# Performance work log

Hardware: AMD Instinct MI355X
Metric: run time of the kernel (lower is better)

The kernel has to match this reference:

```python
import jax, jax.numpy as jnp
import numpy as np

T, B, A, OBS = 128, 16, 32, 256
K, NACT, HID = 3, 9, 32


def setup_inputs() -> dict:
    key = jax.random.key(0)
    ks = jax.random.split(key, 12)
    sc = 0.1  # small init scale for stability
    d = {}
    d["x"] = jax.random.normal(ks[0], (T, B, A, OBS), jnp.float32)
    d["done"] = jax.random.randint(ks[1], (T, B), 0, 2, jnp.int32)
    d["actions"] = jax.random.randint(ks[2], (T, B, A, K), 0, NACT, jnp.int32)
    d["W1"] = sc * jax.random.normal(ks[3], (128, OBS), jnp.float32)
    d["b1"] = jnp.zeros((128,), jnp.float32)
    d["W2"] = sc * jax.random.normal(ks[4], (128, 128), jnp.float32)
    d["b2"] = jnp.zeros((128,), jnp.float32)
    d["W3"] = sc * jax.random.normal(ks[5], (64, 128), jnp.float32)
    d["b3"] = jnp.zeros((64,), jnp.float32)
    d["Wih"] = sc * jax.random.normal(ks[6], (4 * HID, 64), jnp.float32)
    d["Whh"] = sc * jax.random.normal(ks[7], (4 * HID, HID), jnp.float32)
    d["bih"] = jnp.zeros((4 * HID,), jnp.float32)
    d["bhh"] = jnp.zeros((4 * HID,), jnp.float32)
    d["Wh"] = sc * jax.random.normal(ks[8], (K, NACT, HID), jnp.float32)
    d["bh"] = jnp.zeros((K, NACT), jnp.float32)
    d["h0"] = jnp.zeros((B * A, HID), jnp.float32)
    d["c0"] = jnp.zeros((B * A, HID), jnp.float32)
    return d


def _forward(x, done, actions, W1, b1, W2, b2, W3, b3,
             Wih, Whh, bih, bhh, Wh, bh, h0, c0):
    # MLP trunk: n_obs -> 128 -> 128 -> 64 (tanh, tanh, linear)
    z = jnp.tanh(x @ W1.T + b1)
    z = jnp.tanh(z @ W2.T + b2)
    z = z @ W3.T + b3                       # [T, B, A, 64]
    zf = z.reshape(T, B * A, 64)
    # done[t] repeated per agent (repeat_interleave along batch*agent axis)
    done_f = jnp.repeat(done.astype(x.dtype), A, axis=1)  # [T, B*A]

    def step(carry, inp):
        h, c = carry
        zt, dt = inp                        # [B*A,64], [B*A]
        mask = (1.0 - dt)[:, None]
        h = h * mask
        c = c * mask
        gates = zt @ Wih.T + bih + h @ Whh.T + bhh  # [B*A, 4H]
        i, f, g, o = jnp.split(gates, 4, axis=-1)   # PyTorch gate order i,f,g,o
        i, f, o = jax.nn.sigmoid(i), jax.nn.sigmoid(f), jax.nn.sigmoid(o)
        g = jnp.tanh(g)
        c = f * c + i * g
        h = o * jnp.tanh(c)
        return (h, c), h

    (_, _), ys = jax.lax.scan(step, (h0, c0), (zf, done_f))
    y = ys.reshape(T, B, A, HID)
    # multi-head categorical logits: stacked heads [K, NACT, HID]
    logits = jnp.einsum('tbah,knh->tbakn', y, Wh) + bh  # [T,B,A,K,NACT]
    lp = jax.nn.log_softmax(logits, axis=-1)
    entropies = -jnp.sum(jnp.exp(lp) * lp, axis=-1)     # [T,B,A,K]
    alp = jnp.take_along_axis(lp, actions[..., None], axis=-1)[..., 0]  # [T,B,A,K]
    logprobs = jnp.prod(alp, axis=-1)  # faithful: product of per-head log-probs
    return logprobs, entropies


def reference(x, done, actions, W1, b1, W2, b2, W3, b3,
              Wih, Whh, bih, bhh, Wh, bh, h0, c0):
    logprobs, entropies = _forward(x, done, actions, W1, b1, W2, b2, W3, b3,
                                   Wih, Whh, bih, bhh, Wh, bh, h0, c0)
    return actions, logprobs, entropies
```

## Files before the change

### kernel.cpp

```cpp
#include <hip/hip_runtime.h>
#include <math.h>

namespace {
constexpr int Tn = 128, Bn = 16, An = 32, OBS = 256, Kh = 3, NACT = 9, HID = 32;
constexpr int TBA = Tn * Bn * An;
constexpr int BA  = Bn * An;
constexpr int OUT_LP  = TBA * Kh;
constexpr int OUT_ENT = TBA * Kh + TBA;
constexpr int NCHUNK = 32;
constexpr int CHUNKW = Tn / NCHUNK;

typedef __fp16   pk16x2 __attribute__((ext_vector_type(2)));
typedef _Float16 half8v __attribute__((ext_vector_type(8)));
typedef float    f32x4  __attribute__((ext_vector_type(4)));
}

__device__ __forceinline__ float fast_sig(float x) {
  return __builtin_amdgcn_rcpf(1.f + __expf(-x));
}
__device__ __forceinline__ float fast_tanh(float x) {
  return fmaf(2.f, fast_sig(2.f * x), -1.f);
}
__device__ __forceinline__ unsigned h2bits(pk16x2 h) {
  return __builtin_bit_cast(unsigned, h);
}
__device__ __forceinline__ pk16x2 bits2h(unsigned u) {
  return __builtin_bit_cast(pk16x2, u);
}
__device__ __forceinline__ int first_done_ge(unsigned long long dm0,
                                             unsigned long long dm1, int n) {
  unsigned long long m0 = (n < 64) ? (dm0 & (~0ull << n)) : 0ull;
  unsigned long long m1 = (n < 64) ? dm1 : (dm1 & (~0ull << (n - 64)));
  if (m0) return __builtin_ctzll(m0);
  if (m1) return 64 + __builtin_ctzll(m1);
  return 128;
}
__device__ __forceinline__ void bmax3(float& m0, float& m1, float& m2,
                                      int km, float v) {
  m0 = (km == 0) ? fmaxf(m0, v) : m0;
  m1 = (km == 1) ? fmaxf(m1, v) : m1;
  m2 = (km == 2) ? fmaxf(m2, v) : m2;
}
__device__ __forceinline__ void badd3(float& s0, float& s1, float& s2,
                                      int km, float v) {
  s0 += (km == 0) ? v : 0.f;
  s1 += (km == 1) ? v : 0.f;
  s2 += (km == 2) ? v : 0.f;
}
__device__ __forceinline__ float bsel3(float x0, float x1, float x2, int km) {
  return (km == 0) ? x0 : ((km == 1) ? x1 : x2);
}
__device__ __forceinline__ int bseli3(int x0, int x1, int x2, int km) {
  return (km == 0) ? x0 : ((km == 1) ? x1 : x2);
}

template<int ROWS, int WSTR>
__device__ __forceinline__ void stage_whf(const float* __restrict__ Wg, int kofs,
                                          _Float16* __restrict__ wt, int tid)
{
#pragma unroll
  for (int it = 0; it < ROWS/64; ++it) {
    int idx = tid + it*512;
    int o = idx >> 3, g8 = idx & 7;
    const float* p = &Wg[(size_t)o*WSTR + kofs + g8*8];
    float4 c0 = *(const float4*)p;
    float4 c1 = *(const float4*)(p + 4);
    half8v hv = { (_Float16)c0.x, (_Float16)c0.y, (_Float16)c0.z, (_Float16)c0.w,
                  (_Float16)c1.x, (_Float16)c1.y, (_Float16)c1.z, (_Float16)c1.w };
    *(half8v*)&wt[o*72 + g8*8] = hv;
  }
}

template<int NOC, int XSTR>
__device__ __forceinline__ void mfma_slab(const _Float16* __restrict__ xsrc,
                                          const _Float16* __restrict__ wt,
                                          int rA, int ln, int quad, f32x4 acc[8])
{
#pragma unroll
  for (int kc = 0; kc < 2; ++kc) {
    half8v a = *(const half8v*)&xsrc[rA*XSTR + kc*32 + quad*8];
#pragma unroll
    for (int oc = 0; oc < NOC; ++oc) {
      half8v b = *(const half8v*)&wt[(oc*16 + ln)*72 + kc*32 + quad*8];
      acc[oc] = __builtin_amdgcn_mfma_f32_16x16x32_f16(a, b, acc[oc], 0, 0, 0);
    }
  }
}

template<int NOC>
__device__ __forceinline__ void mfma_regA(half8v a0, half8v a1,
                                          const _Float16* __restrict__ wt,
                                          int ln, int quad, f32x4 acc[8])
{
#pragma unroll
  for (int oc = 0; oc < NOC; ++oc) {
    half8v b = *(const half8v*)&wt[(oc*16 + ln)*72 + quad*8];
    acc[oc] = __builtin_amdgcn_mfma_f32_16x16x32_f16(a0, b, acc[oc], 0, 0, 0);
  }
#pragma unroll
  for (int oc = 0; oc < NOC; ++oc) {
    half8v b = *(const half8v*)&wt[(oc*16 + ln)*72 + 32 + quad*8];
    acc[oc] = __builtin_amdgcn_mfma_f32_16x16x32_f16(a1, b, acc[oc], 0, 0, 0);
  }
}

__global__ __launch_bounds__(512, 4) void mlp_kernel(
    const float* __restrict__ x,
    const float* __restrict__ W1, const float* __restrict__ W2,
    const float* __restrict__ W3, const float* __restrict__ Wih,
    const float* __restrict__ b1, const float* __restrict__ b2,
    const float* __restrict__ b3, const float* __restrict__ bih,
    const float* __restrict__ bhh, uint2* __restrict__ G1q)
{
  __shared__ __align__(16) _Float16 wt0[128*72];
  __shared__ __align__(16) _Float16 wt1[128*72];
  __shared__ __align__(16) _Float16 act[128*136];
  const int tid  = threadIdx.x;
  const int w    = tid >> 6;
  const int lane = tid & 63;
  const int ln   = lane & 15;
  const int quad = lane >> 4;
  const int rA   = 16*w + ln;
  const int r0   = 16*w + quad*4;
  const int R0   = blockIdx.x * 128;
  f32x4 acc[8];
  const float* xrow = &x[(size_t)(R0 + rA)*OBS + quad*8];

#define XLOAD(KT, U0, U1, U2, U3) {                                   \
    const float* xp_ = xrow + (KT)*64;                                \
    U0 = *(const float4*)(xp_);      U1 = *(const float4*)(xp_ + 4);  \
    U2 = *(const float4*)(xp_ + 32); U3 = *(const float4*)(xp_ + 36); }
#define XCVT(U0, U1, U2, U3, A0, A1) {                                         \
    A0 = (half8v){(_Float16)U0.x,(_Float16)U0.y,(_Float16)U0.z,(_Float16)U0.w, \
                  (_Float16)U1.x,(_Float16)U1.y,(_Float16)U1.z,(_Float16)U1.w};\
    A1 = (half8v){(_Float16)U2.x,(_Float16)U2.y,(_Float16)U2.z,(_Float16)U2.w, \
                  (_Float16)U3.x,(_Float16)U3.y,(_Float16)U3.z,(_Float16)U3.w}; }

  float4 u0, u1, u2, u3, v0, v1, v2, v3;
  half8v a0, a1;

  XLOAD(0, u0, u1, u2, u3);
  stage_whf<128, 256>(W1, 0, wt0, tid);
#pragma unroll
  for (int oc = 0; oc < 8; ++oc) acc[oc] = (f32x4)0.f;
  __syncthreads();

  stage_whf<128, 256>(W1, 64, wt1, tid);
  XLOAD(1, v0, v1, v2, v3);
  XCVT(u0, u1, u2, u3, a0, a1);
  mfma_regA<8>(a0, a1, wt0, ln, quad, acc);
  __syncthreads();

  stage_whf<128, 256>(W1, 128, wt0, tid);
  XLOAD(2, u0, u1, u2, u3);
  XCVT(v0, v1, v2, v3, a0, a1);
  mfma_regA<8>(a0, a1, wt1, ln, quad, acc);
  __syncthreads();

  stage_whf<128, 256>(W1, 192, wt1, tid);
  XLOAD(3, v0, v1, v2, v3);
  XCVT(u0, u1, u2, u3, a0, a1);
  mfma_regA<8>(a0, a1, wt0, ln, quad, acc);
  __syncthreads();

  stage_whf<128, 128>(W2, 0, wt0, tid);
  XCVT(v0, v1, v2, v3, a0, a1);
  mfma_regA<8>(a0, a1, wt1, ln, quad, acc);
  __syncthreads();

#pragma unroll
  for (int oc = 0; oc < 8; ++oc) {
    int o = oc*16 + ln;
    float bv = b1[o];
#pragma unroll
    for (int r = 0; r < 4; ++r)
      act[(r0 + r)*136 + o] = (_Float16)fast_tanh(acc[oc][r] + bv);
  }

#pragma unroll
  for (int oc = 0; oc < 8; ++oc) acc[oc] = (f32x4)0.f;
  stage_whf<128, 128>(W2, 64, wt1, tid);
  mfma_slab<8, 136>(act, wt0, rA, ln, quad, acc);
  __syncthreads();

  stage_whf<64, 128>(W3, 0, wt0, tid);
  mfma_slab<8, 136>(act + 64, wt1, rA, ln, quad, acc);
  __syncthreads();

#pragma unroll
  for (int oc = 0; oc < 8; ++oc) {
    int o = oc*16 + ln;
    float bv = b2[o];
#pragma unroll
    for (int r = 0; r < 4; ++r)
      act[(r0 + r)*136 + o] = (_Float16)fast_tanh(acc[oc][r] + bv);
  }

#pragma unroll
  for (int oc = 0; oc < 4; ++oc) acc[oc] = (f32x4)0.f;
  stage_whf<64, 128>(W3, 64, wt1, tid);
  mfma_slab<4, 136>(act, wt0, rA, ln, quad, acc);
  __syncthreads();

  stage_whf<128, 64>(Wih, 0, wt0, tid);
  mfma_slab<4, 136>(act + 64, wt1, rA, ln, quad, acc);
  __syncthreads();

#pragma unroll
  for (int oc = 0; oc < 4; ++oc) {
    int o = oc*16 + ln;
    float bv = b3[o];
#pragma unroll
    for (int r = 0; r < 4; ++r)
      act[(r0 + r)*136 + o] = (_Float16)(acc[oc][r] + bv);
  }

#pragma unroll
  for (int oc = 0; oc < 8; ++oc) acc[oc] = (f32x4)0.f;
  mfma_slab<8, 136>(act, wt0, rA, ln, quad, acc);
#pragma unroll
  for (int p = 0; p < 2; ++p) {
    int ui = p*16 + ln;
    float bi = bih[ui]      + bhh[ui];
    float bf = bih[ui + 32] + bhh[ui + 32];
    float bg = bih[ui + 64] + bhh[ui + 64];
    float bo = bih[ui + 96] + bhh[ui + 96];
#pragma unroll
    for (int r = 0; r < 4; ++r) {
      int n = R0 + r0 + r;
      uint2 q;
      q.x = h2bits(__builtin_amdgcn_cvt_pkrtz(acc[p  ][r] + bi, acc[p+4][r] + bg));
      q.y = h2bits(__builtin_amdgcn_cvt_pkrtz(acc[p+2][r] + bf, acc[p+6][r] + bo));
      G1q[(size_t)n*32 + ui] = q;
    }
  }
#undef XLOAD
#undef XCVT
}

__global__ __launch_bounds__(64) void lstm_kernel(
    const uint2* __restrict__ G1q, const float* __restrict__ Whh,
    const float* __restrict__ Wh, const float* __restrict__ bh,
    const int* __restrict__ done, const int* __restrict__ actions,
    const float* __restrict__ h0, const float* __restrict__ c0,
    float* __restrict__ out)
{
  static_assert(BA == 512 && NCHUNK == 32, "index math below assumes 512x32");
  const int lane = threadIdx.x;
  const int ln   = lane & 15;
  const int q    = lane >> 4;
  const int rg   = blockIdx.x & 31;
  const int ck   = blockIdx.x >> 5;
  const int R0   = rg * 16;
  const int b    = R0 >> 5;

  const unsigned long long dm0 = __ballot(done[lane*Bn + b] != 0);
  const unsigned long long dm1 = __ballot(done[(lane + 64)*Bn + b] != 0);

  const int s = (ck == 0) ? 0 : first_done_ge(dm0, dm1, ck * CHUNKW);
  const int e = (ck == NCHUNK - 1) ? Tn
                                   : first_done_ge(dm0, dm1, (ck + 1) * CHUNKW);
  if (s >= e) return;

#define WFRAG(DST, ROWBASE, SRC, STRIDE, SCALE) {                              \
    const float* p_ = &(SRC)[(size_t)((ROWBASE) + ln)*(STRIDE) + q*8];         \
    float4 c0_ = *(const float4*)p_;                                           \
    float4 c1_ = *(const float4*)(p_ + 4);                                     \
    DST = (half8v){                                                            \
      (_Float16)(c0_.x*(SCALE)), (_Float16)(c0_.y*(SCALE)),                    \
      (_Float16)(c0_.z*(SCALE)), (_Float16)(c0_.w*(SCALE)),                    \
      (_Float16)(c1_.x*(SCALE)), (_Float16)(c1_.y*(SCALE)),                    \
      (_Float16)(c1_.z*(SCALE)), (_Float16)(c1_.w*(SCALE))}; }

  half8v wA0, wA1, wA2, wA3, wA4, wA5, wA6, wA7;
  WFRAG(wA0,   0, Whh, HID, 1.f)  WFRAG(wA1,  16, Whh, HID, 1.f)
  WFRAG(wA2,  32, Whh, HID, 1.f)  WFRAG(wA3,  48, Whh, HID, 1.f)
  WFRAG(wA4,  64, Whh, HID, 1.f)  WFRAG(wA5,  80, Whh, HID, 1.f)
  WFRAG(wA6,  96, Whh, HID, 1.f)  WFRAG(wA7, 112, Whh, HID, 1.f)

  half8v whA0, whA1;
  WFRAG(whA0, 0, Wh, HID, 1.f)
  {
    int row = 16 + ln;
    int rc  = (row < 27) ? row : 0;
    float zf = (row < 27) ? 1.f : 0.f;
    const float* p_ = &Wh[(size_t)rc*HID + q*8];
    float4 c0_ = *(const float4*)p_;
    float4 c1_ = *(const float4*)(p_ + 4);
    whA1 = (half8v){
      (_Float16)(c0_.x*zf), (_Float16)(c0_.y*zf),
      (_Float16)(c0_.z*zf), (_Float16)(c0_.w*zf),
      (_Float16)(c1_.x*zf), (_Float16)(c1_.y*zf),
      (_Float16)(c1_.z*zf), (_Float16)(c1_.w*zf)};
  }

  f32x4 bc0, bc1;
#pragma unroll
  for (int r = 0; r < 4; ++r) {
    int m0 = 4*q + r;
    int m1 = 16 + 4*q + r;
    bc0[r] = bh[m0];
    bc1[r] = (m1 < 27) ? bh[m1] : -1e30f;
  }

#define KOF(M, K, O) int K = (M)/9; K = (K > 2) ? 2 : K; const int O = (M) - 9*K;
  const int mA = 4*q, mB = 16 + 4*q;
  KOF(mA+0, kA0, oA0) KOF(mA+1, kA1, oA1) KOF(mA+2, kA2, oA2) KOF(mA+3, kA3, oA3)
  KOF(mB+0, kB0, oB0) KOF(mB+1, kB1, oB1) KOF(mB+2, kB2, oB2) KOF(mB+3, kB3, oB3)
#undef KOF

  const float4 z4 = {0.f, 0.f, 0.f, 0.f};
  float4 cs0, cs1;
  unsigned w0, w1, w2, w3;
  if (ck == 0) {
    const float* hp = &h0[(size_t)(R0 + ln)*HID + 4*q];
    const float* cp = &c0[(size_t)(R0 + ln)*HID + 4*q];
    float4 ha = *(const float4*)hp;
    float4 hb = *(const float4*)(hp + 16);
    cs0 = *(const float4*)cp;
    cs1 = *(const float4*)(cp + 16);
    w0 = h2bits(__builtin_amdgcn_cvt_pkrtz(ha.x, ha.y));
    w1 = h2bits(__builtin_amdgcn_cvt_pkrtz(ha.z, ha.w));
    w2 = h2bits(__builtin_amdgcn_cvt_pkrtz(hb.x, hb.y));
    w3 = h2bits(__builtin_amdgcn_cvt_pkrtz(hb.z, hb.w));
  } else {
    cs0 = z4; cs1 = z4;
    w0 = w1 = w2 = w3 = 0u;
  }

  const int aA = (ln + ((q & 1) << 5)) << 2;
  const int aB = aA + (16 << 2);
  const bool loq = (q < 2);

#define BBUILD(DST) {                                                      \
    unsigned e0_ = (unsigned)__builtin_amdgcn_ds_bpermute(aA, (int)w0);    \
    unsigned e1_ = (unsigned)__builtin_amdgcn_ds_bpermute(aA, (int)w1);    \
    unsigned e2_ = (unsigned)__builtin_amdgcn_ds_bpermute(aA, (int)w2);    \
    unsigned e3_ = (unsigned)__builtin_amdgcn_ds_bpermute(aA, (int)w3);    \
    unsigned o0_ = (unsigned)__builtin_amdgcn_ds_bpermute(aB, (int)w0);    \
    unsigned o1_ = (unsigned)__builtin_amdgcn_ds_bpermute(aB, (int)w1);    \
    unsigned o2_ = (unsigned)__builtin_amdgcn_ds_bpermute(aB, (int)w2);    \
    unsigned o3_ = (unsigned)__builtin_amdgcn_ds_bpermute(aB, (int)w3);    \
    uint4 bu_;                                                             \
    bu_.x = loq ? e0_ : e2_;  bu_.y = loq ? e1_ : e3_;                     \
    bu_.z = loq ? o0_ : o2_;  bu_.w = loq ? o1_ : o3_;                     \
    DST = __builtin_bit_cast(half8v, bu_); }

  half8v Bprev;
  if (ck == 0) { BBUILD(Bprev) }
  else {
    uint4 zz; zz.x = zz.y = zz.z = zz.w = 0u;
    Bprev = __builtin_bit_cast(half8v, zz);
  }

  const uint2* gb = G1q + ((size_t)(R0 + ln) * 32 + 4*q);
  const size_t gstep = (size_t)BA * 32;

#define LOADG(T, A0, A1, A2, A3)                                  \
  { const uint2* p_ = gb + (size_t)(T) * gstep;                   \
    A0 = *(const uint4*)(p_);      A1 = *(const uint4*)(p_ + 2);  \
    A2 = *(const uint4*)(p_ + 16); A3 = *(const uint4*)(p_ + 18); }

  uint4 rc0, rc1, rc2, rc3;
  LOADG(s, rc0, rc1, rc2, rc3);

  for (int t = s; t < e; ++t) {
    int tn = (t + 1 < e) ? t + 1 : e - 1;
    uint4 rn0, rn1, rn2, rn3;
    LOADG(tn, rn0, rn1, rn2, rn3);

    const int rowG = t*BA + R0 + ln;
    const int* ap = actions + (size_t)rowG*3;
    int a0 = ap[0], a1 = ap[1], a2 = ap[2];

    unsigned long long dbit = (t < 64) ? (dm0 >> t) : (dm1 >> (t - 64));
    half8v Buse = Bprev;
    if (dbit & 1ull) {
      uint4 zz; zz.x = zz.y = zz.z = zz.w = 0u;
      Buse = __builtin_bit_cast(half8v, zz);
      cs0 = z4; cs1 = z4;
    }

    f32x4 ci0, cf0, cg0, co0, ci1, cf1, cg1, co1;
    {
      pk16x2 ig, fo;
      ig = bits2h(rc0.x); fo = bits2h(rc0.y);
      ci0[0] = ig.x; cg0[0] = ig.y; cf0[0] = fo.x; co0[0] = fo.y;
      ig = bits2h(rc0.z); fo = bits2h(rc0.w);
      ci0[1] = ig.x; cg0[1] = ig.y; cf0[1] = fo.x; co0[1] = fo.y;
      ig = bits2h(rc1.x); fo = bits2h(rc1.y);
      ci0[2] = ig.x; cg0[2] = ig.y; cf0[2] = fo.x; co0[2] = fo.y;
      ig = bits2h(rc1.z); fo = bits2h(rc1.w);
      ci0[3] = ig.x; cg0[3] = ig.y; cf0[3] = fo.x; co0[3] = fo.y;
      ig = bits2h(rc2.x); fo = bits2h(rc2.y);
      ci1[0] = ig.x; cg1[0] = ig.y; cf1[0] = fo.x; co1[0] = fo.y;
      ig = bits2h(rc2.z); fo = bits2h(rc2.w);
      ci1[1] = ig.x; cg1[1] = ig.y; cf1[1] = fo.x; co1[1] = fo.y;
      ig = bits2h(rc3.x); fo = bits2h(rc3.y);
      ci1[2] = ig.x; cg1[2] = ig.y; cf1[2] = fo.x; co1[2] = fo.y;
      ig = bits2h(rc3.z); fo = bits2h(rc3.w);
      ci1[3] = ig.x; cg1[3] = ig.y; cf1[3] = fo.x; co1[3] = fo.y;
    }

    f32x4 ai0 = __builtin_amdgcn_mfma_f32_16x16x32_f16(wA0, Buse, ci0, 0, 0, 0);
    f32x4 ai1 = __builtin_amdgcn_mfma_f32_16x16x32_f16(wA1, Buse, ci1, 0, 0, 0);
    f32x4 af0 = __builtin_amdgcn_mfma_f32_16x16x32_f16(wA2, Buse, cf0, 0, 0, 0);
    f32x4 af1 = __builtin_amdgcn_mfma_f32_16x16x32_f16(wA3, Buse, cf1, 0, 0, 0);
    f32x4 ag0 = __builtin_amdgcn_mfma_f32_16x16x32_f16(wA4, Buse, cg0, 0, 0, 0);
    f32x4 ag1 = __builtin_amdgcn_mfma_f32_16x16x32_f16(wA5, Buse, cg1, 0, 0, 0);
    f32x4 ao0 = __builtin_amdgcn_mfma_f32_16x16x32_f16(wA6, Buse, co0, 0, 0, 0);
    f32x4 ao1 = __builtin_amdgcn_mfma_f32_16x16x32_f16(wA7, Buse, co1, 0, 0, 0);

    f32x4 hva, hvb;
#pragma unroll
    for (int r = 0; r < 4; ++r) {
      float iv = fast_sig(ai0[r]);
      float fv = fast_sig(af0[r]);
      float gv = fast_tanh(ag0[r]);
      float ov = fast_sig(ao0[r]);
      float cc = fmaf(fv, cs0[r], iv * gv);
      cs0[r] = cc;
      hva[r] = ov * fast_tanh(cc);
    }
#pragma unroll
    for (int r = 0; r < 4; ++r) {
      float iv = fast_sig(ai1[r]);
      float fv = fast_sig(af1[r]);
      float gv = fast_tanh(ag1[r]);
      float ov = fast_sig(ao1[r]);
      float cc = fmaf(fv, cs1[r], iv * gv);
      cs1[r] = cc;
      hvb[r] = ov * fast_tanh(cc);
    }

    w0 = h2bits(__builtin_amdgcn_cvt_pkrtz(hva[0], hva[1]));
    w1 = h2bits(__builtin_amdgcn_cvt_pkrtz(hva[2], hva[3]));
    w2 = h2bits(__builtin_amdgcn_cvt_pkrtz(hvb[0], hvb[1]));
    w3 = h2bits(__builtin_amdgcn_cvt_pkrtz(hvb[2], hvb[3]));
    BBUILD(Bprev)

    f32x4 lh0 = __builtin_amdgcn_mfma_f32_16x16x32_f16(whA0, Bprev, bc0, 0, 0, 0);
    f32x4 lh1 = __builtin_amdgcn_mfma_f32_16x16x32_f16(whA1, Bprev, bc1, 0, 0, 0);

    float mx0 = -1e30f, mx1 = -1e30f, mx2 = -1e30f;
    bmax3(mx0, mx1, mx2, kA0, lh0[0]); bmax3(mx0, mx1, mx2, kA1, lh0[1]);
    bmax3(mx0, mx1, mx2, kA2, lh0[2]); bmax3(mx0, mx1, mx2, kA3, lh0[3]);
    bmax3(mx0, mx1, mx2, kB0, lh1[0]); bmax3(mx0, mx1, mx2, kB1, lh1[1]);
    bmax3(mx0, mx1, mx2, kB2, lh1[2]); bmax3(mx0, mx1, mx2, kB3, lh1[3]);
    mx0 = fmaxf(mx0, __shfl_xor(mx0, 16)); mx0 = fmaxf(mx0, __shfl_xor(mx0, 32));
    mx1 = fmaxf(mx1, __shfl_xor(mx1, 16)); mx1 = fmaxf(mx1, __shfl_xor(mx1, 32));
    mx2 = fmaxf(mx2, __shfl_xor(mx2, 16)); mx2 = fmaxf(mx2, __shfl_xor(mx2, 32));

    float ev0 = __expf(lh0[0] - bsel3(mx0, mx1, mx2, kA0));
    float ev1 = __expf(lh0[1] - bsel3(mx0, mx1, mx2, kA1));
    float ev2 = __expf(lh0[2] - bsel3(mx0, mx1, mx2, kA2));
    float ev3 = __expf(lh0[3] - bsel3(mx0, mx1, mx2, kA3));
    float ev4 = __expf(lh1[0] - bsel3(mx0, mx1, mx2, kB0));
    float ev5 = __expf(lh1[1] - bsel3(mx0, mx1, mx2, kB1));
    float ev6 = __expf(lh1[2] - bsel3(mx0, mx1, mx2, kB2));
    float ev7 = __expf(lh1[3] - bsel3(mx0, mx1, mx2, kB3));
    float s0 = 0.f, s1 = 0.f, s2 = 0.f;
    badd3(s0, s1, s2, kA0, ev0); badd3(s0, s1, s2, kA1, ev1);
    badd3(s0, s1, s2, kA2, ev2); badd3(s0, s1, s2, kA3, ev3);
    badd3(s0, s1, s2, kB0, ev4); badd3(s0, s1, s2, kB1, ev5);
    badd3(s0, s1, s2, kB2, ev6); badd3(s0, s1, s2, kB3, ev7);
    s0 += __shfl_xor(s0, 16); s0 += __shfl_xor(s0, 32);
    s1 += __shfl_xor(s1, 16); s1 += __shfl_xor(s1, 32);
    s2 += __shfl_xor(s2, 16); s2 += __shfl_xor(s2, 32);
    float lse0 = mx0 + __logf(s0);
    float lse1 = mx1 + __logf(s1);
    float lse2 = mx2 + __logf(s2);
    float sc0 = __expf(mx0 - lse0);
    float sc1 = __expf(mx1 - lse1);
    float sc2 = __expf(mx2 - lse2);

    float en0 = 0.f, en1 = 0.f, en2 = 0.f;
    float pl = 1.f;
#define HSLOT(LV, EV, KM, OM) {                                \
      float lse_ = bsel3(lse0, lse1, lse2, KM);                \
      float lp_  = (LV) - lse_;                                \
      float p_   = (EV) * bsel3(sc0, sc1, sc2, KM);            \
      badd3(en0, en1, en2, KM, -p_ * lp_);                     \
      int a_ = bseli3(a0, a1, a2, KM);                         \
      pl = ((OM) == a_) ? pl * lp_ : pl; }
    HSLOT(lh0[0], ev0, kA0, oA0) HSLOT(lh0[1], ev1, kA1, oA1)
    HSLOT(lh0[2], ev2, kA2, oA2) HSLOT(lh0[3], ev3, kA3, oA3)
    HSLOT(lh1[0], ev4, kB0, oB0) HSLOT(lh1[1], ev5, kB1, oB1)
    HSLOT(lh1[2], ev6, kB2, oB2) HSLOT(lh1[3], ev7, kB3, oB3)
#undef HSLOT
    en0 += __shfl_xor(en0, 16); en0 += __shfl_xor(en0, 32);
    en1 += __shfl_xor(en1, 16); en1 += __shfl_xor(en1, 32);
    en2 += __shfl_xor(en2, 16); en2 += __shfl_xor(en2, 32);
    pl  *= __shfl_xor(pl, 16);  pl  *= __shfl_xor(pl, 32);

    if (q == 0) {
      float* ob = out + (size_t)rowG*3;
      ob[0] = (float)a0; ob[1] = (float)a1; ob[2] = (float)a2;
      float* eb = out + OUT_ENT + (size_t)rowG*3;
      eb[0] = en0; eb[1] = en1; eb[2] = en2;
      out[OUT_LP + rowG] = pl;
    }

    rc0 = rn0; rc1 = rn1; rc2 = rn2; rc3 = rn3;
  }
#undef LOADG
#undef BBUILD
#undef WFRAG
}

extern "C" void kernel_launch(void* const* d_in, const int* in_sizes, int n_in,
                              void* d_out, int out_size, void* d_ws, size_t ws_size,
                              hipStream_t stream)
{
  const float* x       = (const float*)d_in[0];
  const int*   done    = (const int*)  d_in[1];
  const int*   actions = (const int*)  d_in[2];
  const float* W1  = (const float*)d_in[3];
  const float* b1  = (const float*)d_in[4];
  const float* W2  = (const float*)d_in[5];
  const float* b2  = (const float*)d_in[6];
  const float* W3  = (const float*)d_in[7];
  const float* b3  = (const float*)d_in[8];
  const float* Wih = (const float*)d_in[9];
  const float* Whh = (const float*)d_in[10];
  const float* bih = (const float*)d_in[11];
  const float* bhh = (const float*)d_in[12];
  const float* Wh  = (const float*)d_in[13];
  const float* bh  = (const float*)d_in[14];
  const float* h0  = (const float*)d_in[15];
  const float* c0  = (const float*)d_in[16];
  float* out = (float*)d_out;

  uint2* G1q = (uint2*)d_ws;

  mlp_kernel<<<TBA/128, 512, 0, stream>>>(
      x, W1, W2, W3, Wih, b1, b2, b3, bih, bhh, G1q);
  lstm_kernel<<<32 * NCHUNK, 64, 0, stream>>>(
      G1q, Whh, Wh, bh, done, actions, h0, c0, out);
}
```

Before: 168.2 us.

## Fuse MLP and LSTM kernels with per-block release/acquire flags

Merges the MLP projection kernel and the chunked LSTM kernel into one launch of 512 blocks. Each block first computes its 128 rows of input gates, then publishes a release flag, and two of its waves take over LSTM chunks, spin-waiting on the flags of the time steps they need. The aim is to remove the second launch and the full-grid barrier between the stages so that recurrence chunks can start while other blocks are still in the MLP. In exchange it adds a memset, spin-wait traffic and a risk of deadlock if not all blocks are co-resident, and most LSTM threads sit idle in 512-thread blocks.

Result: slower. 310.3 us (+84.6%).

```diff
diff --git a/kernel.cpp b/kernel.cpp
--- a/kernel.cpp
+++ b/kernel.cpp
@@ -104,27 +104,35 @@
   }
 }
 
-__global__ __launch_bounds__(512, 4) void mlp_kernel(
+__global__ __launch_bounds__(512, 4) void fused_kernel(
     const float* __restrict__ x,
     const float* __restrict__ W1, const float* __restrict__ W2,
     const float* __restrict__ W3, const float* __restrict__ Wih,
     const float* __restrict__ b1, const float* __restrict__ b2,
     const float* __restrict__ b3, const float* __restrict__ bih,
-    const float* __restrict__ bhh, uint2* __restrict__ G1q)
+    const float* __restrict__ bhh,
+    const float* __restrict__ Whh, const float* __restrict__ Wh,
+    const float* __restrict__ bhd, const int* __restrict__ done,
+    const int* __restrict__ actions, const float* __restrict__ h0,
+    const float* __restrict__ c0,
+    uint2* __restrict__ G1q, unsigned* __restrict__ flags,
+    float* __restrict__ out)
 {
   __shared__ __align__(16) _Float16 wt0[128*72];
   __shared__ __align__(16) _Float16 wt1[128*72];
   __shared__ __align__(16) _Float16 act[128*136];
-  const int tid  = threadIdx.x;
-  const int w    = tid >> 6;
-  const int lane = tid & 63;
-  const int ln   = lane & 15;
-  const int quad = lane >> 4;
-  const int rA   = 16*w + ln;
-  const int r0   = 16*w + quad*4;
-  const int R0   = blockIdx.x * 128;
-  f32x4 acc[8];
-  const float* xrow = &x[(size_t)(R0 + rA)*OBS + quad*8];
+  const int tid = threadIdx.x;
+
+  {
+    const int w    = tid >> 6;
+    const int lane = tid & 63;
+    const int ln   = lane & 15;
+    const int quad = lane >> 4;
+    const int rA   = 16*w + ln;
+    const int r0   = 16*w + quad*4;
+    const int R0   = blockIdx.x * 128;
+    f32x4 acc[8];
+    const float* xrow = &x[(size_t)(R0 + rA)*OBS + quad*8];
 
 #define XLOAD(KT, U0, U1, U2, U3) {                                   \
     const float* xp_ = xrow + (KT)*64;                                \
@@ -136,121 +144,122 @@
     A1 = (half8v){(_Float16)U2.x,(_Float16)U2.y,(_Float16)U2.z,(_Float16)U2.w, \
                   (_Float16)U3.x,(_Float16)U3.y,(_Float16)U3.z,(_Float16)U3.w}; }
 
-  float4 u0, u1, u2, u3, v0, v1, v2, v3;
-  half8v a0, a1;
-
-  XLOAD(0, u0, u1, u2, u3);
-  stage_whf<128, 256>(W1, 0, wt0, tid);
-#pragma unroll
-  for (int oc = 0; oc < 8; ++oc) acc[oc] = (f32x4)0.f;
-  __syncthreads();
-
-  stage_whf<128, 256>(W1, 64, wt1, tid);
-  XLOAD(1, v0, v1, v2, v3);
-  XCVT(u0, u1, u2, u3, a0, a1);
-  mfma_regA<8>(a0, a1, wt0, ln, quad, acc);
-  __syncthreads();
-
-  stage_whf<128, 256>(W1, 128, wt0, tid);
-  XLOAD(2, u0, u1, u2, u3);
-  XCVT(v0, v1, v2, v3, a0, a1);
-  mfma_regA<8>(a0, a1, wt1, ln, quad, acc);
-  __syncthreads();
-
-  stage_whf<128, 256>(W1, 192, wt1, tid);
-  XLOAD(3, v0, v1, v2, v3);
-  XCVT(u0, u1, u2, u3, a0, a1);
-  mfma_regA<8>(a0, a1, wt0, ln, quad, acc);
-  __syncthreads();
-
-  stage_whf<128, 128>(W2, 0, wt0, tid);
-  XCVT(v0, v1, v2, v3, a0, a1);
-  mfma_regA<8>(a0, a1, wt1, ln, quad, acc);
-  __syncthreads();
-
-#pragma unroll
-  for (int oc = 0; oc < 8; ++oc) {
-    int o = oc*16 + ln;
-    float bv = b1[o];
-#pragma unroll
-    for (int r = 0; r < 4; ++r)
-      act[(r0 + r)*136 + o] = (_Float16)fast_tanh(acc[oc][r] + bv);
-  }
-
-#pragma unroll
-  for (int oc = 0; oc < 8; ++oc) acc[oc] = (f32x4)0.f;
-  stage_whf<128, 128>(W2, 64, wt1, tid);
-  mfma_slab<8, 136>(act, wt0, rA, ln, quad, acc);
-  __syncthreads();
-
-  stage_whf<64, 128>(W3, 0, wt0, tid);
-  mfma_slab<8, 136>(act + 64, wt1, rA, ln, quad, acc);
-  __syncthreads();
-
-#pragma unroll
-  for (int oc = 0; oc < 8; ++oc) {
-    int o = oc*16 + ln;
-    float bv = b2[o];
-#pragma unroll
-    for (int r = 0; r < 4; ++r)
-      act[(r0 + r)*136 + o] = (_Float16)fast_tanh(acc[oc][r] + bv);
-  }
-
-#pragma unroll
-  for (int oc = 0; oc < 4; ++oc) acc[oc] = (f32x4)0.f;
-  stage_whf<64, 128>(W3, 64, wt1, tid);
-  mfma_slab<4, 136>(act, wt0, rA, ln, quad, acc);
-  __syncthreads();
-
-  stage_whf<128, 64>(Wih, 0, wt0, tid);
-  mfma_slab<4, 136>(act + 64, wt1, rA, ln, quad, acc);
-  __syncthreads();
-
-#pragma unroll
-  for (int oc = 0; oc < 4; ++oc) {
-    int o = oc*16 + ln;
-    float bv = b3[o];
-#pragma unroll
-    for (int r = 0; r < 4; ++r)
-      act[(r0 + r)*136 + o] = (_Float16)(acc[oc][r] + bv);
-  }
-
-#pragma unroll
-  for (int oc = 0; oc < 8; ++oc) acc[oc] = (f32x4)0.f;
-  mfma_slab<8, 136>(act, wt0, rA, ln, quad, acc);
-#pragma unroll
-  for (int p = 0; p < 2; ++p) {
-    int ui = p*16 + ln;
-    float bi = bih[ui]      + bhh[ui];
-    float bf = bih[ui + 32] + bhh[ui + 32];
-    float bg = bih[ui + 64] + bhh[ui + 64];
-    float bo = bih[ui + 96] + bhh[ui + 96];
-#pragma unroll
-    for (int r = 0; r < 4; ++r) {
-      int n = R0 + r0 + r;
-      uint2 q;
-      q.x = h2bits(__builtin_amdgcn_cvt_pkrtz(acc[p  ][r] + bi, acc[p+4][r] + bg));
-      q.y = h2bits(__builtin_amdgcn_cvt_pkrtz(acc[p+2][r] + bf, acc[p+6][r] + bo));
-      G1q[(size_t)n*32 + ui] = q;
-    }
-  }
+    float4 u0, u1, u2, u3, v0, v1, v2, v3;
+    half8v a0, a1;
+
+    XLOAD(0, u0, u1, u2, u3);
+    stage_whf<128, 256>(W1, 0, wt0, tid);
+#pragma unroll
+    for (int oc = 0; oc < 8; ++oc) acc[oc] = (f32x4)0.f;
+    __syncthreads();
+
+    stage_whf<128, 256>(W1, 64, wt1, tid);
+    XLOAD(1, v0, v1, v2, v3);
+    XCVT(u0, u1, u2, u3, a0, a1);
+    mfma_regA<8>(a0, a1, wt0, ln, quad, acc);
+    __syncthreads();
+
+    stage_whf<128, 256>(W1, 128, wt0, tid);
+    XLOAD(2, u0, u1, u2, u3);
+    XCVT(v0, v1, v2, v3, a0, a1);
+    mfma_regA<8>(a0, a1, wt1, ln, quad, acc);
+    __syncthreads();
+
+    stage_whf<128, 256>(W1, 192, wt1, tid);
+    XLOAD(3, v0, v1, v2, v3);
+    XCVT(u0, u1, u2, u3, a0, a1);
+    mfma_regA<8>(a0, a1, wt0, ln, quad, acc);
+    __syncthreads();
+
+    stage_whf<128, 128>(W2, 0, wt0, tid);
+    XCVT(v0, v1, v2, v3, a0, a1);
+    mfma_regA<8>(a0, a1, wt1, ln, quad, acc);
+    __syncthreads();
+
+#pragma unroll
+    for (int oc = 0; oc < 8; ++oc) {
+      int o = oc*16 + ln;
+      float bv = b1[o];
+#pragma unroll
+      for (int r = 0; r < 4; ++r)
+        act[(r0 + r)*136 + o] = (_Float16)fast_tanh(acc[oc][r] + bv);
+    }
+
+#pragma unroll
+    for (int oc = 0; oc < 8; ++oc) acc[oc] = (f32x4)0.f;
+    stage_whf<128, 128>(W2, 64, wt1, tid);
+    mfma_slab<8, 136>(act, wt0, rA, ln, quad, acc);
+    __syncthreads();
+
+    stage_whf<64, 128>(W3, 0, wt0, tid);
+    mfma_slab<8, 136>(act + 64, wt1, rA, ln, quad, acc);
+    __syncthreads();
+
+#pragma unroll
+    for (int oc = 0; oc < 8; ++oc) {
+      int o = oc*16 + ln;
+      float bv = b2[o];
+#pragma unroll
+      for (int r = 0; r < 4; ++r)
+        act[(r0 + r)*136 + o] = (_Float16)fast_tanh(acc[oc][r] + bv);
+    }
+
+#pragma unroll
+    for (int oc = 0; oc < 4; ++oc) acc[oc] = (f32x4)0.f;
+    stage_whf<64, 128>(W3, 64, wt1, tid);
+    mfma_slab<4, 136>(act, wt0, rA, ln, quad, acc);
+    __syncthreads();
+
+    stage_whf<128, 64>(Wih, 0, wt0, tid);
+    mfma_slab<4, 136>(act + 64, wt1, rA, ln, quad, acc);
+    __syncthreads();
+
+#pragma unroll
+    for (int oc = 0; oc < 4; ++oc) {
+      int o = oc*16 + ln;
+      float bv = b3[o];
+#pragma unroll
+      for (int r = 0; r < 4; ++r)
+        act[(r0 + r)*136 + o] = (_Float16)(acc[oc][r] + bv);
+    }
+
+#pragma unroll
+    for (int oc = 0; oc < 8; ++oc) acc[oc] = (f32x4)0.f;
+    mfma_slab<8, 136>(act, wt0, rA, ln, quad, acc);
+#pragma unroll
+    for (int p = 0; p < 2; ++p) {
+      int ui = p*16 + ln;
+      float bi = bih[ui]      + bhh[ui];
+      float bf = bih[ui + 32] + bhh[ui + 32];
+      float bg = bih[ui + 64] + bhh[ui + 64];
+      float bo = bih[ui + 96] + bhh[ui + 96];
+#pragma unroll
+      for (int r = 0; r < 4; ++r) {
+        int n = R0 + r0 + r;
+        uint2 qv;
+        qv.x = h2bits(__builtin_amdgcn_cvt_pkrtz(acc[p  ][r] + bi, acc[p+4][r] + bg));
+        qv.y = h2bits(__builtin_amdgcn_cvt_pkrtz(acc[p+2][r] + bf, acc[p+6][r] + bo));
+        G1q[(size_t)n*32 + ui] = qv;
+      }
+    }
 #undef XLOAD
 #undef XCVT
-}
-
-__global__ __launch_bounds__(64) void lstm_kernel(
-    const uint2* __restrict__ G1q, const float* __restrict__ Whh,
-    const float* __restrict__ Wh, const float* __restrict__ bh,
-    const int* __restrict__ done, const int* __restrict__ actions,
-    const float* __restrict__ h0, const float* __restrict__ c0,
-    float* __restrict__ out)
-{
-  static_assert(BA == 512 && NCHUNK == 32, "index math below assumes 512x32");
-  const int lane = threadIdx.x;
+  }
+
+  __threadfence();
+  __syncthreads();
+  if (tid == 0)
+    __hip_atomic_store(&flags[blockIdx.x], 1u, __ATOMIC_RELEASE,
+                       __HIP_MEMORY_SCOPE_AGENT);
+
+  const int wv = tid >> 6;
+  if (wv >= 2) return;
+  const int lane = tid & 63;
   const int ln   = lane & 15;
   const int q    = lane >> 4;
-  const int rg   = blockIdx.x & 31;
-  const int ck   = blockIdx.x >> 5;
+  const int u    = blockIdx.x * 2 + wv;
+  const int rg   = u & 31;
+  const int ck   = u >> 5;
   const int R0   = rg * 16;
   const int b    = R0 >> 5;
 
@@ -262,24 +271,22 @@
                                    : first_done_ge(dm0, dm1, (ck + 1) * CHUNKW);
   if (s >= e) return;
 
-#define WFRAG(DST, ROWBASE, SRC, STRIDE, SCALE) {                              \
+#define WFRAG(DST, ROWBASE, SRC, STRIDE) {                                     \
     const float* p_ = &(SRC)[(size_t)((ROWBASE) + ln)*(STRIDE) + q*8];         \
     float4 c0_ = *(const float4*)p_;                                           \
     float4 c1_ = *(const float4*)(p_ + 4);                                     \
     DST = (half8v){                                                            \
-      (_Float16)(c0_.x*(SCALE)), (_Float16)(c0_.y*(SCALE)),                    \
-      (_Float16)(c0_.z*(SCALE)), (_Float16)(c0_.w*(SCALE)),                    \
-      (_Float16)(c1_.x*(SCALE)), (_Float16)(c1_.y*(SCALE)),                    \
-      (_Float16)(c1_.z*(SCALE)), (_Float16)(c1_.w*(SCALE))}; }
+      (_Float16)c0_.x, (_Float16)c0_.y, (_Float16)c0_.z, (_Float16)c0_.w,     \
+      (_Float16)c1_.x, (_Float16)c1_.y, (_Float16)c1_.z, (_Float16)c1_.w}; }
 
   half8v wA0, wA1, wA2, wA3, wA4, wA5, wA6, wA7;
-  WFRAG(wA0,   0, Whh, HID, 1.f)  WFRAG(wA1,  16, Whh, HID, 1.f)
-  WFRAG(wA2,  32, Whh, HID, 1.f)  WFRAG(wA3,  48, Whh, HID, 1.f)
-  WFRAG(wA4,  64, Whh, HID, 1.f)  WFRAG(wA5,  80, Whh, HID, 1.f)
-  WFRAG(wA6,  96, Whh, HID, 1.f)  WFRAG(wA7, 112, Whh, HID, 1.f)
+  WFRAG(wA0,   0, Whh, HID)  WFRAG(wA1,  16, Whh, HID)
+  WFRAG(wA2,  32, Whh, HID)  WFRAG(wA3,  48, Whh, HID)
+  WFRAG(wA4,  64, Whh, HID)  WFRAG(wA5,  80, Whh, HID)
+  WFRAG(wA6,  96, Whh, HID)  WFRAG(wA7, 112, Whh, HID)
 
   half8v whA0, whA1;
-  WFRAG(whA0, 0, Wh, HID, 1.f)
+  WFRAG(whA0, 0, Wh, HID)
   {
     int row = 16 + ln;
     int rc  = (row < 27) ? row : 0;
@@ -293,14 +300,15 @@
       (_Float16)(c1_.x*zf), (_Float16)(c1_.y*zf),
       (_Float16)(c1_.z*zf), (_Float16)(c1_.w*zf)};
   }
+#undef WFRAG
 
   f32x4 bc0, bc1;
 #pragma unroll
   for (int r = 0; r < 4; ++r) {
     int m0 = 4*q + r;
     int m1 = 16 + 4*q + r;
-    bc0[r] = bh[m0];
-    bc1[r] = (m1 < 27) ? bh[m1] : -1e30f;
+    bc0[r] = bhd[m0];
+    bc1[r] = (m1 < 27) ? bhd[m1] : -1e30f;
   }
 
 #define KOF(M, K, O) int K = (M)/9; K = (K > 2) ? 2 : K; const int O = (M) - 9*K;
@@ -351,6 +359,15 @@
   else {
     uint4 zz; zz.x = zz.y = zz.z = zz.w = 0u;
     Bprev = __builtin_bit_cast(half8v, zz);
+  }
+
+  {
+    const int q8 = rg >> 3;
+    for (int tt = s; tt < e; ++tt) {
+      while (__hip_atomic_load(&flags[4*tt + q8], __ATOMIC_ACQUIRE,
+                               __HIP_MEMORY_SCOPE_AGENT) == 0u)
+        __builtin_amdgcn_s_sleep(8);
+    }
   }
 
   const uint2* gb = G1q + ((size_t)(R0 + ln) * 32 + 4*q);
@@ -505,7 +522,6 @@
   }
 #undef LOADG
 #undef BBUILD
-#undef WFRAG
 }
 
 extern "C" void kernel_launch(void* const* d_in, const int* in_sizes, int n_in,
@@ -532,9 +548,10 @@
   float* out = (float*)d_out;
 
   uint2* G1q = (uint2*)d_ws;
-
-  mlp_kernel<<<TBA/128, 512, 0, stream>>>(
-      x, W1, W2, W3, Wih, b1, b2, b3, bih, bhh, G1q);
-  lstm_kernel<<<32 * NCHUNK, 64, 0, stream>>>(
-      G1q, Whh, Wh, bh, done, actions, h0, c0, out);
-}
+  unsigned* flags = (unsigned*)(G1q + (size_t)TBA*32);
+
+  hipMemsetAsync(flags, 0, 512 * sizeof(unsigned), stream);
+  fused_kernel<<<512, 512, 0, stream>>>(
+      x, W1, W2, W3, Wih, b1, b2, b3, bih, bhh,
+      Whh, Wh, bh, done, actions, h0, c0, G1q, flags, out);
+}
```

## Halve MLP block size and single-buffer weight staging to cut LDS use

Applied to the files above, without the earlier changes.

The MLP kernel now runs 64-row blocks of 256 threads instead of 128-row blocks of 512 threads, with twice as many blocks. Weight staging drops from two LDS buffers to one, and the activation buffer shrinks to match. The aim is a smaller per-block shared-memory footprint so more blocks fit per CU. In exchange, staging no longer overlaps with MFMA compute, so each stage needs an extra barrier, and every block reloads all the weights, roughly doubling total weight staging traffic. The LSTM weight-fragment macro is also cleaned up to drop a no-op scale.

Measured after the change: 175.9 us. 1.05x slower.

```diff
diff --git a/kernel.cpp b/kernel.cpp
--- a/kernel.cpp
+++ b/kernel.cpp
@@ -59,8 +59,8 @@
                                           _Float16* __restrict__ wt, int tid)
 {
 #pragma unroll
-  for (int it = 0; it < ROWS/64; ++it) {
-    int idx = tid + it*512;
+  for (int it = 0; it < ROWS/32; ++it) {
+    int idx = tid + it*256;
     int o = idx >> 3, g8 = idx & 7;
     const float* p = &Wg[(size_t)o*WSTR + kofs + g8*8];
     float4 c0 = *(const float4*)p;
@@ -104,7 +104,7 @@
   }
 }
 
-__global__ __launch_bounds__(512, 4) void mlp_kernel(
+__global__ __launch_bounds__(256, 4) void mlp_kernel(
     const float* __restrict__ x,
     const float* __restrict__ W1, const float* __restrict__ W2,
     const float* __restrict__ W3, const float* __restrict__ Wih,
@@ -112,9 +112,8 @@
     const float* __restrict__ b3, const float* __restrict__ bih,
     const float* __restrict__ bhh, uint2* __restrict__ G1q)
 {
-  __shared__ __align__(16) _Float16 wt0[128*72];
-  __shared__ __align__(16) _Float16 wt1[128*72];
-  __shared__ __align__(16) _Float16 act[128*136];
+  __shared__ __align__(16) _Float16 wt[128*72];
+  __shared__ __align__(16) _Float16 act[64*136];
   const int tid  = threadIdx.x;
   const int w    = tid >> 6;
   const int lane = tid & 63;
@@ -122,7 +121,7 @@
   const int quad = lane >> 4;
   const int rA   = 16*w + ln;
   const int r0   = 16*w + quad*4;
-  const int R0   = blockIdx.x * 128;
+  const int R0   = blockIdx.x * 64;
   f32x4 acc[8];
   const float* xrow = &x[(size_t)(R0 + rA)*OBS + quad*8];
 
@@ -139,33 +138,35 @@
   float4 u0, u1, u2, u3, v0, v1, v2, v3;
   half8v a0, a1;
 
+#pragma unroll
+  for (int oc = 0; oc < 8; ++oc) acc[oc] = (f32x4)0.f;
+
   XLOAD(0, u0, u1, u2, u3);
-  stage_whf<128, 256>(W1, 0, wt0, tid);
-#pragma unroll
-  for (int oc = 0; oc < 8; ++oc) acc[oc] = (f32x4)0.f;
-  __syncthreads();
-
-  stage_whf<128, 256>(W1, 64, wt1, tid);
+  stage_whf<128, 256>(W1, 0, wt, tid);
   XLOAD(1, v0, v1, v2, v3);
+  __syncthreads();
   XCVT(u0, u1, u2, u3, a0, a1);
-  mfma_regA<8>(a0, a1, wt0, ln, quad, acc);
-  __syncthreads();
-
-  stage_whf<128, 256>(W1, 128, wt0, tid);
+  mfma_regA<8>(a0, a1, wt, ln, quad, acc);
+  __syncthreads();
+
+  stage_whf<128, 256>(W1, 64, wt, tid);
   XLOAD(2, u0, u1, u2, u3);
+  __syncthreads();
   XCVT(v0, v1, v2, v3, a0, a1);
-  mfma_regA<8>(a0, a1, wt1, ln, quad, acc);
-  __syncthreads();
-
-  stage_whf<128, 256>(W1, 192, wt1, tid);
+  mfma_regA<8>(a0, a1, wt, ln, quad, acc);
+  __syncthreads();
+
+  stage_whf<128, 256>(W1, 128, wt, tid);
   XLOAD(3, v0, v1, v2, v3);
+  __syncthreads();
   XCVT(u0, u1, u2, u3, a0, a1);
-  mfma_regA<8>(a0, a1, wt0, ln, quad, acc);
-  __syncthreads();
-
-  stage_whf<128, 128>(W2, 0, wt0, tid);
+  mfma_regA<8>(a0, a1, wt, ln, quad, acc);
+  __syncthreads();
+
+  stage_whf<128, 256>(W1, 192, wt, tid);
+  __syncthreads();
   XCVT(v0, v1, v2, v3, a0, a1);
-  mfma_regA<8>(a0, a1, wt1, ln, quad, acc);
+  mfma_regA<8>(a0, a1, wt, ln, quad, acc);
   __syncthreads();
 
 #pragma unroll
@@ -179,12 +180,14 @@
 
 #pragma unroll
   for (int oc = 0; oc < 8; ++oc) acc[oc] = (f32x4)0.f;
-  stage_whf<128, 128>(W2, 64, wt1, tid);
-  mfma_slab<8, 136>(act, wt0, rA, ln, quad, acc);
-  __syncthreads();
-
-  stage_whf<64, 128>(W3, 0, wt0, tid);
-  mfma_slab<8, 136>(act + 64, wt1, rA, ln, quad, acc);
+  stage_whf<128, 128>(W2, 0, wt, tid);
+  __syncthreads();
+  mfma_slab<8, 136>(act, wt, rA, ln, quad, acc);
+  __syncthreads();
+
+  stage_whf<128, 128>(W2, 64, wt, tid);
+  __syncthreads();
+  mfma_slab<8, 136>(act + 64, wt, rA, ln, quad, acc);
   __syncthreads();
 
 #pragma unroll
@@ -198,12 +201,14 @@
 
 #pragma unroll
   for (int oc = 0; oc < 4; ++oc) acc[oc] = (f32x4)0.f;
-  stage_whf<64, 128>(W3, 64, wt1, tid);
-  mfma_slab<4, 136>(act, wt0, rA, ln, quad, acc);
-  __syncthreads();
-
-  stage_whf<128, 64>(Wih, 0, wt0, tid);
-  mfma_slab<4, 136>(act + 64, wt1, rA, ln, quad, acc);
+  stage_whf<64, 128>(W3, 0, wt, tid);
+  __syncthreads();
+  mfma_slab<4, 136>(act, wt, rA, ln, quad, acc);
+  __syncthreads();
+
+  stage_whf<64, 128>(W3, 64, wt, tid);
+  __syncthreads();
+  mfma_slab<4, 136>(act + 64, wt, rA, ln, quad, acc);
   __syncthreads();
 
 #pragma unroll
@@ -217,7 +222,9 @@
 
 #pragma unroll
   for (int oc = 0; oc < 8; ++oc) acc[oc] = (f32x4)0.f;
-  mfma_slab<8, 136>(act, wt0, rA, ln, quad, acc);
+  stage_whf<128, 64>(Wih, 0, wt, tid);
+  __syncthreads();
+  mfma_slab<8, 136>(act, wt, rA, ln, quad, acc);
 #pragma unroll
   for (int p = 0; p < 2; ++p) {
     int ui = p*16 + ln;
@@ -228,10 +235,10 @@
 #pragma unroll
     for (int r = 0; r < 4; ++r) {
       int n = R0 + r0 + r;
-      uint2 q;
-      q.x = h2bits(__builtin_amdgcn_cvt_pkrtz(acc[p  ][r] + bi, acc[p+4][r] + bg));
-      q.y = h2bits(__builtin_amdgcn_cvt_pkrtz(acc[p+2][r] + bf, acc[p+6][r] + bo));
-      G1q[(size_t)n*32 + ui] = q;
+      uint2 qv;
+      qv.x = h2bits(__builtin_amdgcn_cvt_pkrtz(acc[p  ][r] + bi, acc[p+4][r] + bg));
+      qv.y = h2bits(__builtin_amdgcn_cvt_pkrtz(acc[p+2][r] + bf, acc[p+6][r] + bo));
+      G1q[(size_t)n*32 + ui] = qv;
     }
   }
 #undef XLOAD
@@ -262,24 +269,22 @@
                                    : first_done_ge(dm0, dm1, (ck + 1) * CHUNKW);
   if (s >= e) return;
 
-#define WFRAG(DST, ROWBASE, SRC, STRIDE, SCALE) {                              \
+#define WFRAG(DST, ROWBASE, SRC, STRIDE) {                                     \
     const float* p_ = &(SRC)[(size_t)((ROWBASE) + ln)*(STRIDE) + q*8];         \
     float4 c0_ = *(const float4*)p_;                                           \
     float4 c1_ = *(const float4*)(p_ + 4);                                     \
     DST = (half8v){                                                            \
-      (_Float16)(c0_.x*(SCALE)), (_Float16)(c0_.y*(SCALE)),                    \
-      (_Float16)(c0_.z*(SCALE)), (_Float16)(c0_.w*(SCALE)),                    \
-      (_Float16)(c1_.x*(SCALE)), (_Float16)(c1_.y*(SCALE)),                    \
-      (_Float16)(c1_.z*(SCALE)), (_Float16)(c1_.w*(SCALE))}; }
+      (_Float16)c0_.x, (_Float16)c0_.y, (_Float16)c0_.z, (_Float16)c0_.w,     \
+      (_Float16)c1_.x, (_Float16)c1_.y, (_Float16)c1_.z, (_Float16)c1_.w}; }
 
   half8v wA0, wA1, wA2, wA3, wA4, wA5, wA6, wA7;
-  WFRAG(wA0,   0, Whh, HID, 1.f)  WFRAG(wA1,  16, Whh, HID, 1.f)
-  WFRAG(wA2,  32, Whh, HID, 1.f)  WFRAG(wA3,  48, Whh, HID, 1.f)
-  WFRAG(wA4,  64, Whh, HID, 1.f)  WFRAG(wA5,  80, Whh, HID, 1.f)
-  WFRAG(wA6,  96, Whh, HID, 1.f)  WFRAG(wA7, 112, Whh, HID, 1.f)
+  WFRAG(wA0,   0, Whh, HID)  WFRAG(wA1,  16, Whh, HID)
+  WFRAG(wA2,  32, Whh, HID)  WFRAG(wA3,  48, Whh, HID)
+  WFRAG(wA4,  64, Whh, HID)  WFRAG(wA5,  80, Whh, HID)
+  WFRAG(wA6,  96, Whh, HID)  WFRAG(wA7, 112, Whh, HID)
 
   half8v whA0, whA1;
-  WFRAG(whA0, 0, Wh, HID, 1.f)
+  WFRAG(whA0, 0, Wh, HID)
   {
     int row = 16 + ln;
     int rc  = (row < 27) ? row : 0;
@@ -293,6 +298,7 @@
       (_Float16)(c1_.x*zf), (_Float16)(c1_.y*zf),
       (_Float16)(c1_.z*zf), (_Float16)(c1_.w*zf)};
   }
+#undef WFRAG
 
   f32x4 bc0, bc1;
 #pragma unroll
@@ -505,7 +511,6 @@
   }
 #undef LOADG
 #undef BBUILD
-#undef WFRAG
 }
 
 extern "C" void kernel_launch(void* const* d_in, const int* in_sizes, int n_in,
@@ -533,7 +538,7 @@
 
   uint2* G1q = (uint2*)d_ws;
 
-  mlp_kernel<<<TBA/128, 512, 0, stream>>>(
+  mlp_kernel<<<TBA/64, 256, 0, stream>>>(
       x, W1, W2, W3, Wih, b1, b2, b3, bih, bhh, G1q);
   lstm_kernel<<<32 * NCHUNK, 64, 0, stream>>>(
       G1q, Whh, Wh, bh, done, actions, h0, c0, out);
```
